# Performance work log

Hardware: AMD Instinct MI355X
Metric: run time of the kernel (lower is better)

## Reference

```python
import jax, jax.numpy as jnp
import numpy as np

VOCAB = 100000
EMB_DIM = 50
KERNEL_NUM = 21
SIGMA = 0.1
EXACT_SIGMA = 0.001

# kernel mus/sigmas exactly as KNRM._get_kernels_layers
_MUS = [(2.0 * (i + 1) - KERNEL_NUM) / (KERNEL_NUM - 1) for i in range(KERNEL_NUM - 1)] + [1.0]
_SIGMAS = [SIGMA] * (KERNEL_NUM - 1) + [EXACT_SIGMA]


def setup_inputs() -> dict:
    key = jax.random.key(0)
    k1, k2, k3, k4, k5, k6, k7 = jax.random.split(key, 7)
    B, Lq, Ld = 1024, 32, 512
    return {
        "query_1": jax.random.randint(k1, (B, Lq), 0, VOCAB),
        "document_1": jax.random.randint(k2, (B, Ld), 0, VOCAB),
        "query_2": jax.random.randint(k3, (B, Lq), 0, VOCAB),
        "document_2": jax.random.randint(k4, (B, Ld), 0, VOCAB),
        "emb": jax.random.normal(k5, (VOCAB, EMB_DIM), dtype=jnp.float32),
        "mlp_w": jax.random.normal(k6, (1, KERNEL_NUM), dtype=jnp.float32) * 0.1,
        "mlp_b": jax.random.normal(k7, (1,), dtype=jnp.float32) * 0.1,
    }


def _predict(q_idx, d_idx, emb, mlp_w, mlp_b):
    q = emb[q_idx]                                   # [B, Lq, E]
    d = emb[d_idx]                                   # [B, Ld, E]
    qn = jnp.linalg.norm(q, axis=2)                  # [B, Lq]
    dn = jnp.linalg.norm(d, axis=2)                  # [B, Ld]
    sim = jnp.einsum('bqe,bde->bqd', q, d)
    sim = sim / (qn[:, :, None] * dn[:, None, :])
    sim = jnp.where(jnp.isnan(sim), 0.0, sim)        # [B, Lq, Ld]
    KM = []
    for mu, s in zip(_MUS, _SIGMAS):
        g = jnp.exp(-(sim - mu) ** 2 / (2.0 * s * s))
        KM.append(jnp.sum(jnp.log1p(jnp.sum(g, axis=-1)), axis=-1))
    kernels_out = jnp.stack(KM, axis=1)              # [B, 21]
    return kernels_out @ mlp_w.T + mlp_b             # [B, 1]


def reference(query_1, document_1, query_2, document_2, emb, mlp_w, mlp_b):
    logits_1 = _predict(query_1, document_1, emb, mlp_w, mlp_b)
    logits_2 = _predict(query_2, document_2, emb, mlp_w, mlp_b)
    return jax.nn.sigmoid(logits_1 - logits_2)
```

## Files before the change

### kernel.cpp

```cpp
#include <hip/hip_runtime.h>
#include <math.h>

#define LOG2E 1.4426950408889634f

typedef __attribute__((ext_vector_type(8))) short    short8;
typedef __attribute__((ext_vector_type(8))) _Float16 half8;
typedef __attribute__((ext_vector_type(4))) float    f32x4;
typedef __attribute__((ext_vector_type(2))) float    f32x2;

__device__ __forceinline__ float fexp2(float x) { return __builtin_amdgcn_exp2f(x); }

typedef __attribute__((address_space(1))) const unsigned int gas_u32;
typedef __attribute__((address_space(3))) unsigned int las_u32;
__device__ __forceinline__ void glds16(const uint4* g, uint4* l)
{ __builtin_amdgcn_global_load_lds((gas_u32*)g, (las_u32*)l, 16, 0, 0); }

__device__ __forceinline__ void kern21(f32x2 s, f32x2* acc)
{
    s.x = __builtin_amdgcn_fmed3f(s.x, -1.1f, 1.1f);
    s.y = __builtin_amdgcn_fmed3f(s.y, -1.1f, 1.1f);

    f32x2 va = s * 14.426950408889634f + 0.7213475204444817f;
    f32x2 v, vi, gc;
    v.x  = fexp2(va.x);  v.y  = fexp2(va.y);
    vi.x = __builtin_amdgcn_rcpf(v.x);
    vi.y = __builtin_amdgcn_rcpf(v.y);
    f32x2 t9 = s + 0.05f;
    f32x2 ga = (t9 * t9) * -72.13475204444817f;
    gc.x = fexp2(ga.x);  gc.y = fexp2(ga.y);

    f32x2 p = gc;
    acc[9] += p;
    #pragma unroll
    for (int k = 10; k <= 19; ++k) { p *= v; acc[k] += p; }
    f32x2 q = gc;
    #pragma unroll
    for (int k = 8; k >= 0; --k) { q *= vi; acc[k] += q; }
    if (__any(fmaxf(s.x, s.y) > 0.995f)) {
        f32x2 te = s - 1.0f;
        f32x2 ea = (te * te) * -721347.5204444817f;
        f32x2 ge; ge.x = fexp2(ea.x); ge.y = fexp2(ea.y);
        acc[20] += ge;
    }
}

__device__ __forceinline__ void doc_step2(
    half8 A0, half8 A1, half8 B0, half8 B1, f32x2* acc)
{
    f32x4 C = {0.f, 0.f, 0.f, 0.f};
    C = __builtin_amdgcn_mfma_f32_16x16x32_f16(A0, B0, C, 0, 0, 0);
    C = __builtin_amdgcn_mfma_f32_16x16x32_f16(A1, B1, C, 0, 0, 0);
    f32x2 a01 = {C[0], C[1]};
    f32x2 a23 = {C[2], C[3]};
    kern21(a01, acc);
    kern21(a23, acc);
}

__global__ __launch_bounds__(256) void knrm_prep_kernel(
    const float* __restrict__ emb, uint4* __restrict__ wse, int vocab)
{
    const int tid = threadIdx.x;
    const int row = blockIdx.x * 32 + (tid >> 3);
    const int cb  = tid & 7;
    if (row >= vocab) return;

    const float* src = emb + (size_t)row * 50;
    float v[8];
    float ss = 0.f;
    #pragma unroll
    for (int p = 0; p < 4; ++p) {
        int e = cb * 8 + 2 * p;
        float2 t;
        if (e + 2 <= 50) t = *(const float2*)(src + e);
        else             t = make_float2(0.f, 0.f);
        v[2*p]   = t.x;
        v[2*p+1] = t.y;
        ss = fmaf(t.x, t.x, fmaf(t.y, t.y, ss));
    }
    ss += __shfl_xor(ss, 1, 64);
    ss += __shfl_xor(ss, 2, 64);
    ss += __shfl_xor(ss, 4, 64);
    float rn = __builtin_amdgcn_rsqf(ss);

    half8 hv;
    #pragma unroll
    for (int p = 0; p < 8; ++p) hv[p] = (_Float16)(v[p] * rn);
    wse[(size_t)row * 8 + cb] = __builtin_bit_cast(uint4, hv);
}

__device__ __forceinline__ half8 frag_ldh(const uint4* mat, int row, int chunk)
{
    return __builtin_bit_cast(half8, mat[row * 8 + (chunk ^ (row & 7))]);
}

__global__ __launch_bounds__(256, 4) void knrm_pass_pre(
    const int* __restrict__ q1, const int* __restrict__ d1,
    const int* __restrict__ q2, const int* __restrict__ d2,
    const uint4* __restrict__ wse, const float* __restrict__ mlp_w,
    float* __restrict__ ws_logit)
{
    __shared__ uint4 dbuf[2][512];
    __shared__ float Swk[4][21][16];
    __shared__ float wred[4];

    const int tid  = threadIdx.x;
    const int bx   = blockIdx.x;
    const int b    = bx >> 1;
    const int lane = tid & 63;
    const int wave = tid >> 6;
    const int g    = lane >> 4;

    const int* qidx = ((bx & 1) ? q2 : q1) + b * 32;
    const int* didx = ((bx & 1) ? d2 : d1) + b * 512;

    const int rsub = lane >> 3;
    const int cpos = lane & 7;
    const int swz  = cpos ^ rsub;

    {
        const int srow = tid >> 3, scb = tid & 7;
        const uint4* sq = wse + (size_t)qidx[srow] * 8;
        int pos = srow * 8 + (scb ^ (srow & 7));
        dbuf[1][pos] = sq[scb];
    }
    {
        const uint4* p0 = wse + (size_t)didx[wave * 16 + rsub] * 8;
        const uint4* p1 = wse + (size_t)didx[wave * 16 + 8 + rsub] * 8;
        glds16(p0 + swz, &dbuf[0][wave * 128]);
        glds16(p1 + swz, &dbuf[0][wave * 128 + 64]);
    }
    int tokA = didx[64 + wave * 16 + rsub];
    int tokB = didx[64 + wave * 16 + 8 + rsub];
    __syncthreads();

    const int qrow = (wave >> 1) * 16 + (lane & 15);
    half8 B0 = frag_ldh(dbuf[1], qrow, g);
    half8 B1 = frag_ldh(dbuf[1], qrow, 4 + g);
    __syncthreads();

    f32x2 acc2[21];
    #pragma unroll
    for (int k = 0; k < 21; ++k) acc2[k] = (f32x2){0.f, 0.f};

    const int ar0 = (wave & 1) * 16 + (lane & 15);
    const int ar1 = 32 + ar0;

    for (int c = 0; c < 8; ++c) {
        if (c < 7) {
            const uint4* pA = wse + (size_t)tokA * 8;
            const uint4* pB = wse + (size_t)tokB * 8;
            uint4* nb = dbuf[(c + 1) & 1];
            glds16(pA + swz, nb + wave * 128);
            glds16(pB + swz, nb + wave * 128 + 64);
            if (c < 6) {
                tokA = didx[(c + 2) * 64 + wave * 16 + rsub];
                tokB = didx[(c + 2) * 64 + wave * 16 + 8 + rsub];
            }
        }
        const uint4* hb = dbuf[c & 1];
        doc_step2(frag_ldh(hb, ar0, g), frag_ldh(hb, ar0, 4 + g), B0, B1, acc2);
        doc_step2(frag_ldh(hb, ar1, g), frag_ldh(hb, ar1, 4 + g), B0, B1, acc2);
        __syncthreads();
    }

    float acc[21];
    #pragma unroll
    for (int k = 0; k < 21; ++k) {
        float v = acc2[k].x + acc2[k].y;
        v += __shfl_xor(v, 16, 64);
        v += __shfl_xor(v, 32, 64);
        acc[k] = v;
    }
    if (lane < 16) {
        #pragma unroll
        for (int k = 0; k < 21; ++k) Swk[wave][k][lane] = acc[k];
    }
    __syncthreads();

    float local = 0.f;
    for (int p = tid; p < 21 * 32; p += 256) {
        int k = p >> 5, q = p & 31;
        int wp = (q >> 4) * 2;
        float S = Swk[wp][k][q & 15] + Swk[wp + 1][k][q & 15];
        float j = (float)(k - 9);
        float scale = (k < 20) ? fexp2(-0.7213475204444817f * j * j) : 1.0f;
        local += mlp_w[k] * log1pf(S * scale);
    }
    #pragma unroll
    for (int off = 1; off < 64; off <<= 1) local += __shfl_xor(local, off, 64);
    if (lane == 0) wred[wave] = local;
    __syncthreads();
    if (tid == 0)
        ws_logit[bx] = wred[0] + wred[1] + wred[2] + wred[3];
}

__device__ __forceinline__ short8 frag_ldb(const uint4* mat, int row, int chunk)
{
    return __builtin_bit_cast(short8, mat[row * 8 + (chunk ^ (row & 7))]);
}

__device__ __forceinline__ void doc_step_fb(
    short8 Ah0, short8 Ah1, short8 Al0, short8 Al1,
    short8 Bh0, short8 Bh1, short8 Bl0, short8 Bl1, f32x2* acc)
{
    f32x4 C = {0.f, 0.f, 0.f, 0.f};
    C = __builtin_amdgcn_mfma_f32_16x16x32_bf16(Ah0, Bh0, C, 0, 0, 0);
    C = __builtin_amdgcn_mfma_f32_16x16x32_bf16(Ah1, Bh1, C, 0, 0, 0);
    C = __builtin_amdgcn_mfma_f32_16x16x32_bf16(Ah0, Bl0, C, 0, 0, 0);
    C = __builtin_amdgcn_mfma_f32_16x16x32_bf16(Ah1, Bl1, C, 0, 0, 0);
    C = __builtin_amdgcn_mfma_f32_16x16x32_bf16(Al0, Bh0, C, 0, 0, 0);
    C = __builtin_amdgcn_mfma_f32_16x16x32_bf16(Al1, Bh1, C, 0, 0, 0);
    f32x2 a01 = {C[0], C[1]};
    f32x2 a23 = {C[2], C[3]};
    kern21(a01, acc);
    kern21(a23, acc);
}

__device__ __forceinline__ void stage_row_chunk(
    const float* __restrict__ emb, int tok, int row, int cb,
    uint4* __restrict__ hmat, uint4* __restrict__ lmat)
{
    const float* src = emb + (size_t)tok * 50;
    float v[8];
    float ss = 0.f;
    #pragma unroll
    for (int p = 0; p < 4; ++p) {
        int e = cb * 8 + 2 * p;
        float2 t;
        if (e + 2 <= 50) t = *(const float2*)(src + e);
        else             t = make_float2(0.f, 0.f);
        v[2*p]   = t.x;
        v[2*p+1] = t.y;
        ss = fmaf(t.x, t.x, fmaf(t.y, t.y, ss));
    }
    ss += __shfl_xor(ss, 1, 64);
    ss += __shfl_xor(ss, 2, 64);
    ss += __shfl_xor(ss, 4, 64);
    float rn = __builtin_amdgcn_rsqf(ss);

    unsigned hw[4], lw[4];
    #pragma unroll
    for (int p = 0; p < 4; ++p) {
        float a = v[2*p]   * rn;
        float b = v[2*p+1] * rn;
        unsigned ha = __float_as_uint(a) & 0xFFFF0000u;
        unsigned hb = __float_as_uint(b) & 0xFFFF0000u;
        float la = a - __uint_as_float(ha);
        float lb = b - __uint_as_float(hb);
        hw[p] = (ha >> 16) | hb;
        lw[p] = (__float_as_uint(la) >> 16) | (__float_as_uint(lb) & 0xFFFF0000u);
    }
    int cidx = cb ^ (row & 7);
    hmat[row * 8 + cidx] = make_uint4(hw[0], hw[1], hw[2], hw[3]);
    lmat[row * 8 + cidx] = make_uint4(lw[0], lw[1], lw[2], lw[3]);
}

__global__ __launch_bounds__(256, 4) void knrm_pass_fb(
    const int* __restrict__ q1, const int* __restrict__ d1,
    const int* __restrict__ q2, const int* __restrict__ d2,
    const float* __restrict__ emb, const float* __restrict__ mlp_w,
    float* __restrict__ ws_logit)
{
    __shared__ uint4 qh4[256], ql4[256];
    __shared__ uint4 dh4[256], dl4[256];
    __shared__ float Swk[4][21][16];
    __shared__ float wred[4];

    const int tid  = threadIdx.x;
    const int bx   = blockIdx.x;
    const int b    = bx >> 1;
    const int lane = tid & 63;
    const int wave = tid >> 6;
    const int g    = lane >> 4;

    const int* qidx = ((bx & 1) ? q2 : q1) + b * 32;
    const int* didx = ((bx & 1) ? d2 : d1) + b * 512;

    const int srow = tid >> 3;
    const int scb  = tid & 7;

    stage_row_chunk(emb, qidx[srow], srow, scb, qh4, ql4);
    __syncthreads();

    const int qrow = (wave >> 1) * 16 + (lane & 15);
    short8 Bh0 = frag_ldb(qh4, qrow, g);
    short8 Bh1 = frag_ldb(qh4, qrow, 4 + g);
    short8 Bl0 = frag_ldb(ql4, qrow, g);
    short8 Bl1 = frag_ldb(ql4, qrow, 4 + g);

    f32x2 acc2[21];
    #pragma unroll
    for (int k = 0; k < 21; ++k) acc2[k] = (f32x2){0.f, 0.f};

    const int arow = (wave & 1) * 16 + (lane & 15);

    for (int c = 0; c < 16; ++c) {
        if (c) __syncthreads();
        stage_row_chunk(emb, didx[c * 32 + srow], srow, scb, dh4, dl4);
        __syncthreads();
        doc_step_fb(frag_ldb(dh4, arow, g), frag_ldb(dh4, arow, 4 + g),
                    frag_ldb(dl4, arow, g), frag_ldb(dl4, arow, 4 + g),
                    Bh0, Bh1, Bl0, Bl1, acc2);
    }
    __syncthreads();

    float acc[21];
    #pragma unroll
    for (int k = 0; k < 21; ++k) {
        float v = acc2[k].x + acc2[k].y;
        v += __shfl_xor(v, 16, 64);
        v += __shfl_xor(v, 32, 64);
        acc[k] = v;
    }
    if (lane < 16) {
        #pragma unroll
        for (int k = 0; k < 21; ++k) Swk[wave][k][lane] = acc[k];
    }
    __syncthreads();

    float local = 0.f;
    for (int p = tid; p < 21 * 32; p += 256) {
        int k = p >> 5, q = p & 31;
        int wp = (q >> 4) * 2;
        float S = Swk[wp][k][q & 15] + Swk[wp + 1][k][q & 15];
        float j = (float)(k - 9);
        float scale = (k < 20) ? fexp2(-0.7213475204444817f * j * j) : 1.0f;
        local += mlp_w[k] * log1pf(S * scale);
    }
    #pragma unroll
    for (int off = 1; off < 64; off <<= 1) local += __shfl_xor(local, off, 64);
    if (lane == 0) wred[wave] = local;
    __syncthreads();
    if (tid == 0)
        ws_logit[bx] = wred[0] + wred[1] + wred[2] + wred[3];
}

__global__ void knrm_final_kernel(const float* __restrict__ P,
                                  float* __restrict__ out, int B)
{
    int i = blockIdx.x * 256 + threadIdx.x;
    if (i < B) {
        float x = P[2 * i] - P[2 * i + 1];
        out[i] = 1.0f / (1.0f + fexp2(-LOG2E * x));
    }
}

extern "C" void kernel_launch(void* const* d_in, const int* in_sizes, int n_in,
                              void* d_out, int out_size, void* d_ws, size_t ws_size,
                              hipStream_t stream) {
    const int*   q1    = (const int*)d_in[0];
    const int*   d1    = (const int*)d_in[1];
    const int*   q2    = (const int*)d_in[2];
    const int*   d2    = (const int*)d_in[3];
    const float* emb   = (const float*)d_in[4];
    const float* mlp_w = (const float*)d_in[5];
    float*       out   = (float*)d_out;

    const int B     = out_size;
    const int vocab = in_sizes[4] / 50;

    float* ws_logit = (float*)d_ws;
    uint4* wse      = (uint4*)((char*)d_ws + 8192);
    size_t need     = 8192 + (size_t)vocab * 128;

    if (ws_size >= need) {
        knrm_prep_kernel<<<dim3((vocab + 31) / 32), dim3(256), 0, stream>>>(emb, wse, vocab);
        knrm_pass_pre<<<dim3(2 * B), dim3(256), 0, stream>>>(
            q1, d1, q2, d2, wse, mlp_w, ws_logit);
    } else {
        knrm_pass_fb<<<dim3(2 * B), dim3(256), 0, stream>>>(
            q1, d1, q2, d2, emb, mlp_w, ws_logit);
    }
    knrm_final_kernel<<<dim3((B + 255) / 256), dim3(256), 0, stream>>>(ws_logit, out, B);
}
```

Baseline: 61.14 us.

## Give each wave private double-buffered doc tiles and drop block barriers

Each wave now loads the document rows it consumes into its own double buffer in shared memory, taking one half of the document, and waits only on its own loads with s_waitcnt instead of block-wide __syncthreads. Query fragments are read straight from global memory into registers, which removes the staging through LDS and its two barriers. This is meant to cut barrier stalls and let waves run independently. The cost is more redundant global query loads and a full vmcnt(0) drain every iteration, which could expose load latency.

Result: no change. 61.38 us (+0.4%).

```diff
diff --git a/kernel.cpp b/kernel.cpp
--- a/kernel.cpp
+++ b/kernel.cpp
@@ -99,7 +99,7 @@
     const uint4* __restrict__ wse, const float* __restrict__ mlp_w,
     float* __restrict__ ws_logit)
 {
-    __shared__ uint4 dbuf[2][512];
+    __shared__ uint4 dbuf[4][2][256];
     __shared__ float Swk[4][21][16];
     __shared__ float wred[4];
 
@@ -111,56 +111,55 @@
     const int g    = lane >> 4;
 
     const int* qidx = ((bx & 1) ? q2 : q1) + b * 32;
-    const int* didx = ((bx & 1) ? d2 : d1) + b * 512;
+    const int* dd   = ((bx & 1) ? d2 : d1) + b * 512 + (wave & 1) * 256;
+
+    const int qrow = (wave >> 1) * 16 + (lane & 15);
+    const uint4* qb = wse + (size_t)qidx[qrow] * 8;
+    half8 B0 = __builtin_bit_cast(half8, qb[g]);
+    half8 B1 = __builtin_bit_cast(half8, qb[4 + g]);
 
     const int rsub = lane >> 3;
-    const int cpos = lane & 7;
-    const int swz  = cpos ^ rsub;
-
-    {
-        const int srow = tid >> 3, scb = tid & 7;
-        const uint4* sq = wse + (size_t)qidx[srow] * 8;
-        int pos = srow * 8 + (scb ^ (srow & 7));
-        dbuf[1][pos] = sq[scb];
-    }
-    {
-        const uint4* p0 = wse + (size_t)didx[wave * 16 + rsub] * 8;
-        const uint4* p1 = wse + (size_t)didx[wave * 16 + 8 + rsub] * 8;
-        glds16(p0 + swz, &dbuf[0][wave * 128]);
-        glds16(p1 + swz, &dbuf[0][wave * 128 + 64]);
-    }
-    int tokA = didx[64 + wave * 16 + rsub];
-    int tokB = didx[64 + wave * 16 + 8 + rsub];
-    __syncthreads();
-
-    const int qrow = (wave >> 1) * 16 + (lane & 15);
-    half8 B0 = frag_ldh(dbuf[1], qrow, g);
-    half8 B1 = frag_ldh(dbuf[1], qrow, 4 + g);
-    __syncthreads();
+    const int swz  = (lane & 7) ^ rsub;
+
+    uint4* buf0 = dbuf[wave][0];
+    uint4* buf1 = dbuf[wave][1];
+
+    int t0 = dd[rsub], t1 = dd[8 + rsub], t2 = dd[16 + rsub], t3 = dd[24 + rsub];
+    glds16(wse + (size_t)t0 * 8 + swz, buf0);
+    glds16(wse + (size_t)t1 * 8 + swz, buf0 + 64);
+    glds16(wse + (size_t)t2 * 8 + swz, buf0 + 128);
+    glds16(wse + (size_t)t3 * 8 + swz, buf0 + 192);
+    t0 = dd[32 + rsub]; t1 = dd[40 + rsub]; t2 = dd[48 + rsub]; t3 = dd[56 + rsub];
 
     f32x2 acc2[21];
     #pragma unroll
     for (int k = 0; k < 21; ++k) acc2[k] = (f32x2){0.f, 0.f};
 
-    const int ar0 = (wave & 1) * 16 + (lane & 15);
-    const int ar1 = 32 + ar0;
+    const int ar0 = lane & 15;
+    const int ar1 = 16 + ar0;
 
     for (int c = 0; c < 8; ++c) {
+        asm volatile("s_waitcnt vmcnt(0)" ::: "memory");
+        __builtin_amdgcn_sched_barrier(0);
+
+        uint4* cur = (c & 1) ? buf1 : buf0;
+        uint4* nxt = (c & 1) ? buf0 : buf1;
+
         if (c < 7) {
-            const uint4* pA = wse + (size_t)tokA * 8;
-            const uint4* pB = wse + (size_t)tokB * 8;
-            uint4* nb = dbuf[(c + 1) & 1];
-            glds16(pA + swz, nb + wave * 128);
-            glds16(pB + swz, nb + wave * 128 + 64);
+            glds16(wse + (size_t)t0 * 8 + swz, nxt);
+            glds16(wse + (size_t)t1 * 8 + swz, nxt + 64);
+            glds16(wse + (size_t)t2 * 8 + swz, nxt + 128);
+            glds16(wse + (size_t)t3 * 8 + swz, nxt + 192);
             if (c < 6) {
-                tokA = didx[(c + 2) * 64 + wave * 16 + rsub];
-                tokB = didx[(c + 2) * 64 + wave * 16 + 8 + rsub];
+                t0 = dd[(c + 2) * 32 + rsub];
+                t1 = dd[(c + 2) * 32 + 8 + rsub];
+                t2 = dd[(c + 2) * 32 + 16 + rsub];
+                t3 = dd[(c + 2) * 32 + 24 + rsub];
             }
         }
-        const uint4* hb = dbuf[c & 1];
-        doc_step2(frag_ldh(hb, ar0, g), frag_ldh(hb, ar0, 4 + g), B0, B1, acc2);
-        doc_step2(frag_ldh(hb, ar1, g), frag_ldh(hb, ar1, 4 + g), B0, B1, acc2);
-        __syncthreads();
+
+        doc_step2(frag_ldh(cur, ar0, g), frag_ldh(cur, ar0, 4 + g), B0, B1, acc2);
+        doc_step2(frag_ldh(cur, ar1, g), frag_ldh(cur, ar1, 4 + g), B0, B1, acc2);
     }
 
     float acc[21];
```
